# Kernel optimization log

Hardware: AMD Instinct MI355X
Metric: run time of the kernel (lower is better)

The kernel has to match this reference:

```python
import jax, jax.numpy as jnp
import numpy as np

V, D, K, NB, T = 50257, 128, 3, 8, 64
DIV_W = 2.0  # diversity_weight


def setup_inputs() -> dict:
    key = jax.random.key(0)
    k1, k2, k3 = jax.random.split(key, 3)
    tokens = jax.random.randint(k1, (T,), 0, V)
    E = jax.random.normal(k2, (V, D), jnp.float32)          # embedding table
    bubbles = 1.5 * jax.random.normal(k3, (K, NB, D), jnp.float32)  # init_spread_foam scale=1.5
    decay_base = jnp.asarray(0.8, jnp.float32)
    sensitivity = jnp.asarray(1.0, jnp.float32)
    return {"tokens": tokens, "E": E, "bubbles": bubbles,
            "decay_base": decay_base, "sensitivity": sensitivity}


def reference(tokens, E, bubbles, decay_base, sensitivity):
    d = E.shape[1]
    inv_sqrt_d = 1.0 / jnp.sqrt(jnp.asarray(d, jnp.float32))
    # normalized bubble states (pure-state directions), fixed over time
    psi = bubbles / (jnp.linalg.norm(bubbles, axis=-1, keepdims=True) + 1e-10)  # [K,NB,D]

    def step(memories, tok):
        # memories: [K, NB, D]
        x = E[tok]  # [D]
        mem_mean = memories.mean(axis=1)  # [K, D]
        mem_norm = jnp.linalg.norm(mem_mean, axis=-1) + 1e-10  # [K]
        x_norm = jnp.linalg.norm(x) + 1e-10
        cos = (mem_mean @ x) / (x_norm * mem_norm)  # [K]
        novelty = jnp.where(mem_norm > 1e-8, 1.0 - cos, 1.0)  # [K]
        decay = jax.nn.sigmoid(decay_base - jnp.abs(sensitivity) * novelty)  # [K]
        xm = x[None, :] + decay[:, None] * mem_mean  # [K, D]

        # foam forward (vectorized over K foams)
        scores = DIV_W * jnp.einsum('knd,kd->kn', bubbles, xm) * inv_sqrt_d  # [K,NB]
        w = jax.nn.softmax(scores, axis=-1)  # [K,NB]
        rho_k = jnp.einsum('kn,knd,kne->kde', w, psi, psi)  # [K,D,D] PSD, trace 1
        eq = w[..., None] * xm[:, None, :] + (1.0 - w)[..., None] * bubbles  # [K,NB,D]
        new_mem = decay[:, None, None] * memories + (1.0 - decay)[:, None, None] * eq

        rho = rho_k.mean(axis=0)  # [D,D] ensemble mixture
        eigs = jnp.clip(jnp.linalg.eigvalsh(rho), 1e-12)
        eigs = eigs / eigs.sum()
        logits = jnp.einsum('vd,de,ve->v', E, rho, E)  # born rule, [V]
        token_probs = jax.nn.softmax(logits)
        S_rho = -(eigs * jnp.clip(jnp.log(eigs), -100.0)).sum()
        H_tokens = -(token_probs * jnp.clip(jnp.log(token_probs), -100.0)).sum()
        F_tokens = H_tokens - S_rho
        logits_k = jnp.einsum('vd,kde,ve->kv', E, rho_k, E)  # [K,V]
        per_foam_probs = jax.nn.softmax(logits_k, axis=-1)
        return new_mem, (token_probs, rho, S_rho, H_tokens, F_tokens, per_foam_probs)

    mem0 = jnp.zeros((bubbles.shape[0], bubbles.shape[1], E.shape[1]), E.dtype)
    _, outs = jax.lax.scan(step, mem0, tokens)
    # outs: token_probs [T,V], rho [T,D,D], S_rho [T], H_tokens [T], F_tokens [T], per_foam_probs [T,K,V]
    return outs
```

## Files before the change

kernel.cpp:

```cpp
#include <hip/hip_runtime.h>
#include <math.h>

namespace {
constexpr int Vv  = 50257;
constexpr int Dc  = 128;
constexpr int Kc  = 3;
constexpr int NBc = 8;
constexpr int Jc  = 24;
constexpr int Tc  = 64;
constexpr int CHV = 1024;
constexpr int NCH = (Vv + CHV - 1) / CHV;
constexpr float INV_SQRT_D = 0.08838834764831845f;
constexpr float DIVW = 2.0f;

constexpr size_t WS_PSI  = 0;
constexpr size_t WS_G    = 4096;
constexpr size_t WS_BB   = 5120;
constexpr size_t WS_XN   = 6144;
constexpr size_t WS_BX   = 6400;
constexpr size_t WS_WALL = 8192;
constexpr size_t WS_PART = 12288;
constexpr size_t WS_LOGZ = 45056;
constexpr size_t WS_P2T  = 65536;

constexpr size_t OFF_TOK = 0;
constexpr size_t OFF_RHO = (size_t)Tc * Vv;
constexpr size_t OFF_S   = OFF_RHO + (size_t)Tc * Dc * Dc;
constexpr size_t OFF_H   = OFF_S + Tc;
constexpr size_t OFF_F   = OFF_H + Tc;
constexpr size_t OFF_PF  = OFF_F + Tc;
}

__device__ __forceinline__ float wsum64(float v) {
#pragma unroll
  for (int m = 1; m < 64; m <<= 1) v += __shfl_xor(v, m);
  return v;
}

__device__ __forceinline__ void comb(float& m1, float& s1, float m2, float s2) {
  float M = fmaxf(m1, m2);
  float e1 = (s1 > 0.f) ? expf(m1 - M) : 0.f;
  float e2 = (s2 > 0.f) ? expf(m2 - M) : 0.f;
  s1 = s1 * e1 + s2 * e2;
  m1 = M;
}
__device__ __forceinline__ void comb_sl(float& m1, float& s1, float& sl1,
                                        float m2, float s2, float sl2) {
  float M = fmaxf(m1, m2);
  float e1 = (s1 > 0.f) ? expf(m1 - M) : 0.f;
  float e2 = (s2 > 0.f) ? expf(m2 - M) : 0.f;
  s1 = s1 * e1 + s2 * e2;
  sl1 = sl1 * e1 + sl2 * e2;
  m1 = M;
}

__device__ __forceinline__ void logits_from_row(const float* __restrict__ p2,
                                                const float* __restrict__ wsh,
                                                int v, float& l0, float& l1, float& l2) {
  const float4* row = (const float4*)(p2 + (size_t)v * Jc);
  float4 q0 = row[0], q1 = row[1], q2 = row[2], q3 = row[3], q4 = row[4], q5 = row[5];
  l0 = 0.f; l1 = 0.f; l2 = 0.f;
  l0 += wsh[0]  * q0.x; l0 += wsh[1]  * q0.y; l0 += wsh[2]  * q0.z; l0 += wsh[3]  * q0.w;
  l0 += wsh[4]  * q1.x; l0 += wsh[5]  * q1.y; l0 += wsh[6]  * q1.z; l0 += wsh[7]  * q1.w;
  l1 += wsh[8]  * q2.x; l1 += wsh[9]  * q2.y; l1 += wsh[10] * q2.z; l1 += wsh[11] * q2.w;
  l1 += wsh[12] * q3.x; l1 += wsh[13] * q3.y; l1 += wsh[14] * q3.z; l1 += wsh[15] * q3.w;
  l2 += wsh[16] * q4.x; l2 += wsh[17] * q4.y; l2 += wsh[18] * q4.z; l2 += wsh[19] * q4.w;
  l2 += wsh[20] * q5.x; l2 += wsh[21] * q5.y; l2 += wsh[22] * q5.z; l2 += wsh[23] * q5.w;
}

__global__ void k_prep(const float* __restrict__ bub, float* __restrict__ ws) {
  __shared__ float braw[Jc * Dc];
  __shared__ float psi[Jc * Dc];
  __shared__ float nrm[Jc];
  int tid = threadIdx.x;
  for (int i = tid; i < Jc * Dc; i += 256) braw[i] = bub[i];
  __syncthreads();
  if (tid < Jc) {
    float s = 0.f;
    for (int d = 0; d < Dc; ++d) { float b = braw[tid * Dc + d]; s += b * b; }
    nrm[tid] = sqrtf(s) + 1e-10f;
  }
  __syncthreads();
  for (int i = tid; i < Jc * Dc; i += 256) {
    float v = braw[i] / nrm[i / Dc];
    psi[i] = v;
    ws[WS_PSI + i] = v;
  }
  __syncthreads();
  for (int i = tid; i < Jc * Jc; i += 256) {
    int r = i / Jc, c = i % Jc;
    float g = 0.f, b = 0.f;
    for (int d = 0; d < Dc; ++d) {
      g += psi[r * Dc + d] * psi[c * Dc + d];
      b += braw[r * Dc + d] * braw[c * Dc + d];
    }
    ws[WS_G + i] = g;
    ws[WS_BB + i] = b;
  }
}

__global__ void k_projtok(const int* __restrict__ tok, const float* __restrict__ E,
                          const float* __restrict__ bub, float* __restrict__ ws) {
  __shared__ float4 psi4[Jc][Dc / 4];
  int bid = blockIdx.x, tid = threadIdx.x;
  if (bid < Tc) {
    if (tid >= 64) return;
    int t = bid, lane = tid;
    int tk = tok[t];
    float eA = E[(size_t)tk * Dc + lane];
    float eB = E[(size_t)tk * Dc + 64 + lane];
    float xn = wsum64(eA * eA + eB * eB);
    if (lane == 0) ws[WS_XN + t] = xn;
    float p[Jc];
#pragma unroll
    for (int j = 0; j < Jc; ++j)
      p[j] = bub[j * Dc + lane] * eA + bub[j * Dc + 64 + lane] * eB;
#pragma unroll
    for (int j = 0; j < Jc; ++j) p[j] = wsum64(p[j]);
    if (lane == 0) {
#pragma unroll
      for (int j = 0; j < Jc; ++j) ws[WS_BX + (size_t)t * Jc + j] = p[j];
    }
    return;
  }
  for (int i = tid; i < Jc * Dc / 4; i += 256)
    ((float4*)psi4)[i] = ((const float4*)(ws + WS_PSI))[i];
  __syncthreads();
  int v = (bid - Tc) * 256 + tid;
  if (v >= Vv) return;
  float acc[Jc];
#pragma unroll
  for (int j = 0; j < Jc; ++j) acc[j] = 0.f;
  const float4* e4 = (const float4*)(E + (size_t)v * Dc);
  for (int d = 0; d < Dc / 4; ++d) {
    float4 e = e4[d];
#pragma unroll
    for (int j = 0; j < Jc; ++j) {
      float4 p = psi4[j][d];
      acc[j] += e.x * p.x + e.y * p.y + e.z * p.z + e.w * p.w;
    }
  }
  float* o = ws + WS_P2T + (size_t)v * Jc;
#pragma unroll
  for (int j = 0; j < Jc; ++j) o[j] = acc[j] * acc[j];
}

__global__ void k_recur(const int* __restrict__ tok, const float* __restrict__ E,
                        const float* __restrict__ bub, const float* __restrict__ pdb,
                        const float* __restrict__ psn, float* __restrict__ ws) {
  __shared__ float sBX[Tc * Jc];
  __shared__ float sXN[Tc];
  int lane = threadIdx.x;
  for (int i = lane; i < Tc * Jc; i += 64) sBX[i] = ws[WS_BX + i];
  if (lane < Tc) sXN[lane] = ws[WS_XN + lane];
  float db = pdb[0];
  float sens = fabsf(psn[0]);
  int tokv = tok[lane];
  float bubA[Jc], bubB[Jc];
#pragma unroll
  for (int j = 0; j < Jc; ++j) {
    bubA[j] = bub[j * Dc + lane];
    bubB[j] = bub[j * Dc + 64 + lane];
  }
  int jme = (lane < Jc) ? lane : (Jc - 1);
  int kme = jme >> 3;
  float BBrow[Jc];
#pragma unroll
  for (int j = 0; j < Jc; ++j) BBrow[j] = ws[WS_BB + (size_t)jme * Jc + j];
  __syncthreads();
  float mmA[Kc] = {0.f, 0.f, 0.f}, mmB[Kc] = {0.f, 0.f, 0.f};
  float BMv[Kc] = {0.f, 0.f, 0.f};
  int tk0 = __shfl(tokv, 0);
  float xA = E[(size_t)tk0 * Dc + lane];
  float xB = E[(size_t)tk0 * Dc + 64 + lane];
  for (int t = 0; t < Tc; ++t) {
    float nxA = 0.f, nxB = 0.f;
    if (t + 1 < Tc) {
      int nk = __shfl(tokv, t + 1);
      nxA = E[(size_t)nk * Dc + lane];
      nxB = E[(size_t)nk * Dc + 64 + lane];
    }
    float dk[Kc], nk2[Kc];
#pragma unroll
    for (int k = 0; k < Kc; ++k) {
      dk[k]  = wsum64(mmA[k] * xA + mmB[k] * xB);
      nk2[k] = wsum64(mmA[k] * mmA[k] + mmB[k] * mmB[k]);
    }
    float xn = sqrtf(sXN[t]) + 1e-10f;
    float dec[Kc], xmA[Kc], xmB[Kc];
#pragma unroll
    for (int k = 0; k < Kc; ++k) {
      float mn = sqrtf(nk2[k]) + 1e-10f;
      float cosv = dk[k] / (xn * mn);
      float nov = (mn > 1e-8f) ? (1.f - cosv) : 1.f;
      dec[k] = 1.f / (1.f + expf(-(db - sens * nov)));
      xmA[k] = xA + dec[k] * mmA[k];
      xmB[k] = xB + dec[k] * mmB[k];
    }
    float bxj = sBX[t * Jc + jme];
    float decS = (kme == 0) ? dec[0] : ((kme == 1) ? dec[1] : dec[2]);
    float sc = (bxj + decS * BMv[kme]) * (DIVW * INV_SQRT_D);
    float mx = sc;
    mx = fmaxf(mx, __shfl_xor(mx, 1));
    mx = fmaxf(mx, __shfl_xor(mx, 2));
    mx = fmaxf(mx, __shfl_xor(mx, 4));
    float e = expf(sc - mx);
    float ss = e;
    ss += __shfl_xor(ss, 1);
    ss += __shfl_xor(ss, 2);
    ss += __shfl_xor(ss, 4);
    float w = e / ss;
    if (lane < Jc) ws[WS_WALL + (size_t)t * Jc + lane] = w;
    float wj[Jc];
#pragma unroll
    for (int j = 0; j < Jc; ++j) wj[j] = __shfl(w, j);
#pragma unroll
    for (int k = 0; k < Kc; ++k) {
      float accA = 0.f, accB = 0.f;
#pragma unroll
      for (int n = 0; n < NBc; ++n) {
        float om = 1.f - wj[k * NBc + n];
        accA += om * bubA[k * NBc + n];
        accB += om * bubB[k * NBc + n];
      }
      float od8 = (1.f - dec[k]) * 0.125f;
      mmA[k] = dec[k] * mmA[k] + od8 * (xmA[k] + accA);
      mmB[k] = dec[k] * mmB[k] + od8 * (xmB[k] + accB);
    }
#pragma unroll
    for (int k = 0; k < Kc; ++k) {
      float bxm = bxj + dec[k] * BMv[k];
      float s2 = 0.f;
#pragma unroll
      for (int n = 0; n < NBc; ++n) s2 += (1.f - wj[k * NBc + n]) * BBrow[k * NBc + n];
      BMv[k] = dec[k] * BMv[k] + (1.f - dec[k]) * 0.125f * (bxm + s2);
    }
    xA = nxA; xB = nxB;
  }
}

__global__ void k_main(float* __restrict__ ws, float* __restrict__ out) {
  __shared__ float sh[Jc * Dc];
  __shared__ float wsh[Jc];
  __shared__ float rm[4][4], rs[4][4], rsl2[4];
  int bid = blockIdx.x, tid = threadIdx.x;

  if (bid < Tc) {
    if (tid >= 64) return;
    int t = bid, lane = tid;
    float* A = sh;
    for (int i = lane; i < Jc * Jc; i += 64) {
      int r = i / Jc, c = i % Jc;
      A[r * 25 + c] = ws[WS_G + i] *
                      sqrtf(ws[WS_WALL + (size_t)t * Jc + r] * ws[WS_WALL + (size_t)t * Jc + c]) *
                      (1.f / 3.f);
    }
    __builtin_amdgcn_wave_barrier();
    for (int sweep = 0; sweep < 7; ++sweep) {
      for (int rr = 0; rr < 23; ++rr) {
        float cv = 1.f, sv = 0.f;
        if (lane < Jc) {
          int j = lane;
          int m = (j == 23) ? rr : ((j == rr) ? 23 : (2 * rr + 23 - j) % 23);
          int lo = min(j, m), hi = max(j, m);
          float ajj = A[j * 25 + j];
          float alh = A[lo * 25 + hi];
          float amm = __shfl(ajj, m);
          float app = (j == lo) ? ajj : amm;
          float aqq = (j == lo) ? amm : ajj;
          if (fabsf(alh) > 1e-20f) {
            float th = (aqq - app) / (2.f * alh);
            float tt = 1.f / (fabsf(th) + sqrtf(1.f + th * th));
            if (th < 0.f) tt = -tt;
            cv = 1.f / sqrtf(1.f + tt * tt);
            sv = tt * cv;
          }
        }
        __builtin_amdgcn_wave_barrier();
#pragma unroll
        for (int it = 0; it < 3; ++it) {
          int b = lane + 64 * it;
          int bb = (b < 144) ? b : 143;
          int pi = bb / 12, pj = bb % 12;
          int p0, q0, p1, q1;
          if (pi == 0) { p0 = rr; q0 = 23; }
          else { int a = (rr + pi) % 23, b2 = (rr + 23 - pi) % 23; p0 = min(a, b2); q0 = max(a, b2); }
          if (pj == 0) { p1 = rr; q1 = 23; }
          else { int a = (rr + pj) % 23, b2 = (rr + 23 - pj) % 23; p1 = min(a, b2); q1 = max(a, b2); }
          float ci = __shfl(cv, p0), si = __shfl(sv, p0);
          float cj = __shfl(cv, p1), sj = __shfl(sv, p1);
          if (b < 144) {
            float m00 = A[p0 * 25 + p1], m01 = A[p0 * 25 + q1];
            float m10 = A[q0 * 25 + p1], m11 = A[q0 * 25 + q1];
            float r00 = ci * m00 - si * m10, r01 = ci * m01 - si * m11;
            float r10 = si * m00 + ci * m10, r11 = si * m01 + ci * m11;
            float o00 = cj * r00 - sj * r01, o01 = sj * r00 + cj * r01;
            float o10 = cj * r10 - sj * r11, o11 = sj * r10 + cj * r11;
            A[p0 * 25 + p1] = o00; A[p0 * 25 + q1] = o01;
            A[q0 * 25 + p1] = o10; A[q0 * 25 + q1] = o11;
          }
        }
        __builtin_amdgcn_wave_barrier();
      }
    }
    float lam = 0.f;
    if (lane < Jc) lam = fmaxf(A[lane * 25 + lane], 1e-12f);
    float tot = lam;
#pragma unroll
    for (int off = 32; off; off >>= 1) tot += __shfl_down(tot, off);
    tot = __shfl(tot, 0);
    tot += (float)(Dc - Jc) * 1e-12f;
    float term = 0.f;
    if (lane < Jc) { float p = lam / tot; term = p * logf(p); }
#pragma unroll
    for (int off = 32; off; off >>= 1) term += __shfl_down(term, off);
    if (lane == 0) {
      float pe = 1e-12f / tot;
      out[OFF_S + t] = -(term + (float)(Dc - Jc) * pe * logf(pe));
    }
    return;
  }

  if (bid < 2 * Tc) {
    int t = bid - Tc;
    float* psis = sh;
    for (int i = tid; i < Jc * Dc; i += 256) psis[i] = ws[WS_PSI + i];
    if (tid < Jc) wsh[tid] = ws[WS_WALL + (size_t)t * Jc + tid] * (1.f / 3.f);
    __syncthreads();
    int d = tid >> 1, eh = (tid & 1) * 64;
    float4 acc[16];
#pragma unroll
    for (int i = 0; i < 16; ++i) acc[i] = make_float4(0.f, 0.f, 0.f, 0.f);
    for (int j = 0; j < Jc; ++j) {
      float a = wsh[j] * psis[j * Dc + d];
      const float4* pr = (const float4*)&psis[j * Dc + eh];
#pragma unroll
      for (int i = 0; i < 16; ++i) {
        float4 p = pr[i];
        acc[i].x += a * p.x; acc[i].y += a * p.y; acc[i].z += a * p.z; acc[i].w += a * p.w;
      }
    }
    float* o = out + OFF_RHO + (size_t)t * Dc * Dc + (size_t)d * Dc + eh;
#pragma unroll
    for (int i = 0; i < 16; ++i) ((float4*)o)[i] = acc[i];
    return;
  }

  int lin = bid - 2 * Tc;
  int t = lin / NCH, ch = lin % NCH;
  if (tid < Jc) wsh[tid] = ws[WS_WALL + (size_t)t * Jc + tid];
  __syncthreads();
  float m[4] = {-INFINITY, -INFINITY, -INFINITY, -INFINITY};
  float s[4] = {0.f, 0.f, 0.f, 0.f};
  float sl = 0.f;
  const float* p2 = ws + WS_P2T;
  for (int r = 0; r < 4; ++r) {
    int v = ch * CHV + r * 256 + tid;
    if (v >= Vv) break;
    float l0, l1, l2;
    logits_from_row(p2, wsh, v, l0, l1, l2);
    float l[4] = { l0, l1, l2, (l0 + l1 + l2) * (1.f / 3.f) };
#pragma unroll
    for (int d = 0; d < 4; ++d) {
      float li = l[d];
      if (li > m[d]) {
        float e = expf(m[d] - li);
        s[d] = s[d] * e + 1.f;
        if (d == 3) sl = sl * e + li;
        m[d] = li;
      } else {
        float e = expf(li - m[d]);
        s[d] += e;
        if (d == 3) sl += e * li;
      }
    }
  }
#pragma unroll
  for (int off = 32; off; off >>= 1) {
#pragma unroll
    for (int d = 0; d < 3; ++d) {
      float om = __shfl_down(m[d], off);
      float os = __shfl_down(s[d], off);
      comb(m[d], s[d], om, os);
    }
    float om = __shfl_down(m[3], off);
    float os = __shfl_down(s[3], off);
    float osl = __shfl_down(sl, off);
    comb_sl(m[3], s[3], sl, om, os, osl);
  }
  int wv = tid >> 6, ln = tid & 63;
  if (ln == 0) {
#pragma unroll
    for (int d = 0; d < 4; ++d) { rm[wv][d] = m[d]; rs[wv][d] = s[d]; }
    rsl2[wv] = sl;
  }
  __syncthreads();
  if (tid == 0) {
    float* part = ws + WS_PART + ((size_t)t * NCH + ch) * 9;
    for (int d = 0; d < 3; ++d) {
      float M = rm[0][d], S = rs[0][d];
      for (int w2 = 1; w2 < 4; ++w2) comb(M, S, rm[w2][d], rs[w2][d]);
      part[d] = M; part[4 + d] = S;
    }
    float M = rm[0][3], S = rs[0][3], SL = rsl2[0];
    for (int w2 = 1; w2 < 4; ++w2) comb_sl(M, S, SL, rm[w2][3], rs[w2][3], rsl2[w2]);
    part[3] = M; part[7] = S; part[8] = SL;
  }
}

__global__ void k_reduce(float* __restrict__ ws, float* __restrict__ out) {
  int t = blockIdx.x, tid = threadIdx.x;
  if (tid < 4) {
    float M = -INFINITY, S = 0.f, SL = 0.f;
    for (int ch = 0; ch < NCH; ++ch) {
      const float* p = ws + WS_PART + ((size_t)t * NCH + ch) * 9;
      if (tid == 3) comb_sl(M, S, SL, p[3], p[7], p[8]);
      else          comb(M, S, p[tid], p[4 + tid]);
    }
    float lz = M + logf(S);
    ws[WS_LOGZ + (size_t)t * 4 + tid] = lz;
    if (tid == 3) {
      float H = lz - SL / S;
      float Srho = out[OFF_S + t];
      out[OFF_H + t] = H;
      out[OFF_F + t] = H - Srho;
    }
  }
}

__global__ void k_norm2(const float* __restrict__ ws, float* __restrict__ out) {
  int ch = blockIdx.x, t = blockIdx.y, tid = threadIdx.x;
  __shared__ float wsh[Jc];
  __shared__ float lzs[4];
  if (tid < Jc) wsh[tid] = ws[WS_WALL + (size_t)t * Jc + tid];
  if (tid >= 32 && tid < 36) lzs[tid - 32] = ws[WS_LOGZ + (size_t)t * 4 + (tid - 32)];
  __syncthreads();
  const float* p2 = ws + WS_P2T;
  for (int r = 0; r < 4; ++r) {
    int v = ch * CHV + r * 256 + tid;
    if (v >= Vv) break;
    float l0, l1, l2;
    logits_from_row(p2, wsh, v, l0, l1, l2);
    float l3 = (l0 + l1 + l2) * (1.f / 3.f);
    out[OFF_TOK + (size_t)t * Vv + v] = expf(l3 - lzs[3]);
    out[OFF_PF + ((size_t)t * Kc + 0) * Vv + v] = expf(l0 - lzs[0]);
    out[OFF_PF + ((size_t)t * Kc + 1) * Vv + v] = expf(l1 - lzs[1]);
    out[OFF_PF + ((size_t)t * Kc + 2) * Vv + v] = expf(l2 - lzs[2]);
  }
}

extern "C" void kernel_launch(void* const* d_in, const int* in_sizes, int n_in,
                              void* d_out, int out_size, void* d_ws, size_t ws_size,
                              hipStream_t stream) {
  const int*   tokens = (const int*)d_in[0];
  const float* E      = (const float*)d_in[1];
  const float* bub    = (const float*)d_in[2];
  const float* pdb    = (const float*)d_in[3];
  const float* psn    = (const float*)d_in[4];
  float* out = (float*)d_out;
  float* ws  = (float*)d_ws;

  k_prep<<<1, 256, 0, stream>>>(bub, ws);
  k_projtok<<<Tc + (Vv + 255) / 256, 256, 0, stream>>>(tokens, E, bub, ws);
  k_recur<<<1, 64, 0, stream>>>(tokens, E, bub, pdb, psn, ws);
  k_main<<<2 * Tc + Tc * NCH, 256, 0, stream>>>(ws, out);
  k_reduce<<<Tc, 64, 0, stream>>>(ws, out);
  k_norm2<<<dim3(NCH, Tc), 256, 0, stream>>>(ws, out);
}
```

Baseline: 445.1 us.

## Merge prep/projection kernels and fold logZ reduction into tiled normalization kernel

Merges the bubble-prep kernel into the vocab projection kernel by having every projection block recompute the normalized psi in shared memory, which removes one launch and a dependency. Removes the separate logZ reduction kernel: each normalization block now recomputes logZ for its group of 8 timesteps. That block stages a 512-token slice of the squared projections in shared memory and reuses it across those timesteps, so P2T is read from global memory far fewer times. The cost is redundant recomputation of psi and of the logZ reductions in every block, plus larger shared-memory use.

```diff
diff --git a/kernel.cpp b/kernel.cpp
--- a/kernel.cpp
+++ b/kernel.cpp
@@ -10,6 +10,10 @@
 constexpr int Tc  = 64;
 constexpr int CHV = 1024;
 constexpr int NCH = (Vv + CHV - 1) / CHV;
+constexpr int NVC = 512;
+constexpr int NNCH = (Vv + NVC - 1) / NVC;
+constexpr int NTG = 8;
+constexpr int TPG = Tc / NTG;
 constexpr float INV_SQRT_D = 0.08838834764831845f;
 constexpr float DIVW = 2.0f;
 
@@ -20,7 +24,6 @@
 constexpr size_t WS_BX   = 6400;
 constexpr size_t WS_WALL = 8192;
 constexpr size_t WS_PART = 12288;
-constexpr size_t WS_LOGZ = 45056;
 constexpr size_t WS_P2T  = 65536;
 
 constexpr size_t OFF_TOK = 0;
@@ -68,44 +71,44 @@
   l2 += wsh[20] * q5.x; l2 += wsh[21] * q5.y; l2 += wsh[22] * q5.z; l2 += wsh[23] * q5.w;
 }
 
-__global__ void k_prep(const float* __restrict__ bub, float* __restrict__ ws) {
-  __shared__ float braw[Jc * Dc];
-  __shared__ float psi[Jc * Dc];
+__global__ void k_setup(const int* __restrict__ tok, const float* __restrict__ E,
+                        const float* __restrict__ bub, float* __restrict__ ws) {
+  __shared__ __align__(16) float braw[Jc * Dc];
+  __shared__ __align__(16) float psi[Jc * Dc];
   __shared__ float nrm[Jc];
-  int tid = threadIdx.x;
-  for (int i = tid; i < Jc * Dc; i += 256) braw[i] = bub[i];
-  __syncthreads();
-  if (tid < Jc) {
-    float s = 0.f;
-    for (int d = 0; d < Dc; ++d) { float b = braw[tid * Dc + d]; s += b * b; }
-    nrm[tid] = sqrtf(s) + 1e-10f;
-  }
-  __syncthreads();
-  for (int i = tid; i < Jc * Dc; i += 256) {
-    float v = braw[i] / nrm[i / Dc];
-    psi[i] = v;
-    ws[WS_PSI + i] = v;
-  }
-  __syncthreads();
-  for (int i = tid; i < Jc * Jc; i += 256) {
-    int r = i / Jc, c = i % Jc;
-    float g = 0.f, b = 0.f;
-    for (int d = 0; d < Dc; ++d) {
-      g += psi[r * Dc + d] * psi[c * Dc + d];
-      b += braw[r * Dc + d] * braw[c * Dc + d];
-    }
-    ws[WS_G + i] = g;
-    ws[WS_BB + i] = b;
-  }
-}
-
-__global__ void k_projtok(const int* __restrict__ tok, const float* __restrict__ E,
-                          const float* __restrict__ bub, float* __restrict__ ws) {
-  __shared__ float4 psi4[Jc][Dc / 4];
   int bid = blockIdx.x, tid = threadIdx.x;
-  if (bid < Tc) {
+
+  if (bid == 0) {
+    for (int i = tid; i < Jc * Dc; i += 256) braw[i] = bub[i];
+    __syncthreads();
+    if (tid < Jc) {
+      float s = 0.f;
+      for (int d = 0; d < Dc; ++d) { float b = braw[tid * Dc + d]; s += b * b; }
+      nrm[tid] = sqrtf(s) + 1e-10f;
+    }
+    __syncthreads();
+    for (int i = tid; i < Jc * Dc; i += 256) {
+      float v = braw[i] / nrm[i / Dc];
+      psi[i] = v;
+      ws[WS_PSI + i] = v;
+    }
+    __syncthreads();
+    for (int i = tid; i < Jc * Jc; i += 256) {
+      int r = i / Jc, c = i % Jc;
+      float g = 0.f, b = 0.f;
+      for (int d = 0; d < Dc; ++d) {
+        g += psi[r * Dc + d] * psi[c * Dc + d];
+        b += braw[r * Dc + d] * braw[c * Dc + d];
+      }
+      ws[WS_G + i] = g;
+      ws[WS_BB + i] = b;
+    }
+    return;
+  }
+
+  if (bid <= Tc) {
     if (tid >= 64) return;
-    int t = bid, lane = tid;
+    int t = bid - 1, lane = tid;
     int tk = tok[t];
     float eA = E[(size_t)tk * Dc + lane];
     float eB = E[(size_t)tk * Dc + 64 + lane];
@@ -123,20 +126,29 @@
     }
     return;
   }
-  for (int i = tid; i < Jc * Dc / 4; i += 256)
-    ((float4*)psi4)[i] = ((const float4*)(ws + WS_PSI))[i];
-  __syncthreads();
-  int v = (bid - Tc) * 256 + tid;
+
+  for (int i = tid; i < Jc * Dc; i += 256) braw[i] = bub[i];
+  __syncthreads();
+  if (tid < Jc) {
+    float s = 0.f;
+    for (int d = 0; d < Dc; ++d) { float b = braw[tid * Dc + d]; s += b * b; }
+    nrm[tid] = sqrtf(s) + 1e-10f;
+  }
+  __syncthreads();
+  for (int i = tid; i < Jc * Dc; i += 256) psi[i] = braw[i] / nrm[i / Dc];
+  __syncthreads();
+  int v = (bid - Tc - 1) * 256 + tid;
   if (v >= Vv) return;
   float acc[Jc];
 #pragma unroll
   for (int j = 0; j < Jc; ++j) acc[j] = 0.f;
   const float4* e4 = (const float4*)(E + (size_t)v * Dc);
+  const float4* p4 = (const float4*)psi;
   for (int d = 0; d < Dc / 4; ++d) {
     float4 e = e4[d];
 #pragma unroll
     for (int j = 0; j < Jc; ++j) {
-      float4 p = psi4[j][d];
+      float4 p = p4[j * (Dc / 4) + d];
       acc[j] += e.x * p.x + e.y * p.y + e.z * p.z + e.w * p.w;
     }
   }
@@ -408,44 +420,79 @@
   }
 }
 
-__global__ void k_reduce(float* __restrict__ ws, float* __restrict__ out) {
-  int t = blockIdx.x, tid = threadIdx.x;
-  if (tid < 4) {
+__global__ void k_norm2(const float* __restrict__ ws, float* __restrict__ out) {
+  __shared__ float p2s[Jc][NVC];
+  __shared__ float wshA[TPG][Jc];
+  __shared__ float lzsA[TPG][4];
+  int chv = blockIdx.x, tg = blockIdx.y, tid = threadIdx.x;
+  int v0 = chv * NVC;
+  int t0 = tg * TPG;
+
+#pragma unroll
+  for (int rr = 0; rr < 2; ++rr) {
+    int vl = tid * 2 + rr;
+    int v = v0 + vl;
+    if (v < Vv) {
+      const float4* row = (const float4*)(ws + WS_P2T + (size_t)v * Jc);
+      float4 q0 = row[0], q1 = row[1], q2 = row[2], q3 = row[3], q4 = row[4], q5 = row[5];
+      p2s[0][vl] = q0.x;  p2s[1][vl] = q0.y;  p2s[2][vl] = q0.z;  p2s[3][vl] = q0.w;
+      p2s[4][vl] = q1.x;  p2s[5][vl] = q1.y;  p2s[6][vl] = q1.z;  p2s[7][vl] = q1.w;
+      p2s[8][vl] = q2.x;  p2s[9][vl] = q2.y;  p2s[10][vl] = q2.z; p2s[11][vl] = q2.w;
+      p2s[12][vl] = q3.x; p2s[13][vl] = q3.y; p2s[14][vl] = q3.z; p2s[15][vl] = q3.w;
+      p2s[16][vl] = q4.x; p2s[17][vl] = q4.y; p2s[18][vl] = q4.z; p2s[19][vl] = q4.w;
+      p2s[20][vl] = q5.x; p2s[21][vl] = q5.y; p2s[22][vl] = q5.z; p2s[23][vl] = q5.w;
+    }
+  }
+  if (tid < TPG * Jc)
+    wshA[tid / Jc][tid % Jc] = ws[WS_WALL + (size_t)(t0 + tid / Jc) * Jc + (tid % Jc)];
+  if (tid >= 192 && tid < 192 + TPG * 4) {
+    int p = tid - 192;
+    int tt = p >> 2, d = p & 3;
+    int t = t0 + tt;
     float M = -INFINITY, S = 0.f, SL = 0.f;
     for (int ch = 0; ch < NCH; ++ch) {
-      const float* p = ws + WS_PART + ((size_t)t * NCH + ch) * 9;
-      if (tid == 3) comb_sl(M, S, SL, p[3], p[7], p[8]);
-      else          comb(M, S, p[tid], p[4 + tid]);
+      const float* pp = ws + WS_PART + ((size_t)t * NCH + ch) * 9;
+      if (d == 3) comb_sl(M, S, SL, pp[3], pp[7], pp[8]);
+      else        comb(M, S, pp[d], pp[4 + d]);
     }
     float lz = M + logf(S);
-    ws[WS_LOGZ + (size_t)t * 4 + tid] = lz;
-    if (tid == 3) {
+    lzsA[tt][d] = lz;
+    if (d == 3 && chv == 0) {
       float H = lz - SL / S;
       float Srho = out[OFF_S + t];
       out[OFF_H + t] = H;
       out[OFF_F + t] = H - Srho;
     }
   }
-}
-
-__global__ void k_norm2(const float* __restrict__ ws, float* __restrict__ out) {
-  int ch = blockIdx.x, t = blockIdx.y, tid = threadIdx.x;
-  __shared__ float wsh[Jc];
-  __shared__ float lzs[4];
-  if (tid < Jc) wsh[tid] = ws[WS_WALL + (size_t)t * Jc + tid];
-  if (tid >= 32 && tid < 36) lzs[tid - 32] = ws[WS_LOGZ + (size_t)t * 4 + (tid - 32)];
-  __syncthreads();
-  const float* p2 = ws + WS_P2T;
-  for (int r = 0; r < 4; ++r) {
-    int v = ch * CHV + r * 256 + tid;
-    if (v >= Vv) break;
-    float l0, l1, l2;
-    logits_from_row(p2, wsh, v, l0, l1, l2);
-    float l3 = (l0 + l1 + l2) * (1.f / 3.f);
-    out[OFF_TOK + (size_t)t * Vv + v] = expf(l3 - lzs[3]);
-    out[OFF_PF + ((size_t)t * Kc + 0) * Vv + v] = expf(l0 - lzs[0]);
-    out[OFF_PF + ((size_t)t * Kc + 1) * Vv + v] = expf(l1 - lzs[1]);
-    out[OFF_PF + ((size_t)t * Kc + 2) * Vv + v] = expf(l2 - lzs[2]);
+  __syncthreads();
+
+  for (int tt = 0; tt < TPG; ++tt) {
+    int t = t0 + tt;
+    float lz0 = lzsA[tt][0], lz1 = lzsA[tt][1], lz2 = lzsA[tt][2], lz3 = lzsA[tt][3];
+#pragma unroll
+    for (int rr = 0; rr < 2; ++rr) {
+      int vl = tid + rr * 256;
+      int v = v0 + vl;
+      if (v >= Vv) continue;
+      float l0 = 0.f, l1 = 0.f, l2 = 0.f;
+      l0 += wshA[tt][0]  * p2s[0][vl];  l0 += wshA[tt][1]  * p2s[1][vl];
+      l0 += wshA[tt][2]  * p2s[2][vl];  l0 += wshA[tt][3]  * p2s[3][vl];
+      l0 += wshA[tt][4]  * p2s[4][vl];  l0 += wshA[tt][5]  * p2s[5][vl];
+      l0 += wshA[tt][6]  * p2s[6][vl];  l0 += wshA[tt][7]  * p2s[7][vl];
+      l1 += wshA[tt][8]  * p2s[8][vl];  l1 += wshA[tt][9]  * p2s[9][vl];
+      l1 += wshA[tt][10] * p2s[10][vl]; l1 += wshA[tt][11] * p2s[11][vl];
+      l1 += wshA[tt][12] * p2s[12][vl]; l1 += wshA[tt][13] * p2s[13][vl];
+      l1 += wshA[tt][14] * p2s[14][vl]; l1 += wshA[tt][15] * p2s[15][vl];
+      l2 += wshA[tt][16] * p2s[16][vl]; l2 += wshA[tt][17] * p2s[17][vl];
+      l2 += wshA[tt][18] * p2s[18][vl]; l2 += wshA[tt][19] * p2s[19][vl];
+      l2 += wshA[tt][20] * p2s[20][vl]; l2 += wshA[tt][21] * p2s[21][vl];
+      l2 += wshA[tt][22] * p2s[22][vl]; l2 += wshA[tt][23] * p2s[23][vl];
+      float l3 = (l0 + l1 + l2) * (1.f / 3.f);
+      out[OFF_TOK + (size_t)t * Vv + v] = expf(l3 - lz3);
+      out[OFF_PF + ((size_t)t * Kc + 0) * Vv + v] = expf(l0 - lz0);
+      out[OFF_PF + ((size_t)t * Kc + 1) * Vv + v] = expf(l1 - lz1);
+      out[OFF_PF + ((size_t)t * Kc + 2) * Vv + v] = expf(l2 - lz2);
+    }
   }
 }
 
@@ -460,10 +507,8 @@
   float* out = (float*)d_out;
   float* ws  = (float*)d_ws;
 
-  k_prep<<<1, 256, 0, stream>>>(bub, ws);
-  k_projtok<<<Tc + (Vv + 255) / 256, 256, 0, stream>>>(tokens, E, bub, ws);
+  k_setup<<<1 + Tc + (Vv + 255) / 256, 256, 0, stream>>>(tokens, E, bub, ws);
   k_recur<<<1, 64, 0, stream>>>(tokens, E, bub, pdb, psn, ws);
   k_main<<<2 * Tc + Tc * NCH, 256, 0, stream>>>(ws, out);
-  k_reduce<<<Tc, 64, 0, stream>>>(ws, out);
-  k_norm2<<<dim3(NCH, Tc), 256, 0, stream>>>(ws, out);
-}
+  k_norm2<<<dim3(NNCH, NTG), 256, 0, stream>>>(ws, out);
+}
```

After: 457.6 us. 2.8% more time.

## Merge prep into projection kernel and fold reduce into final normalize kernel

Applied to the files above, without the earlier changes.

Fuses the single-block prep kernel into the projection kernel: each projection block recomputes the normalized bubble directions locally instead of waiting on a separate launch. The Jacobi eigen-solve and entropy computation move into the final kernel, which also does the global logZ combine. Each normalize block redundantly reduces all chunk partials itself, removing the separate reduce kernel. This cuts six launches to four and removes serial single-block stages, in exchange for redundant per-block recomputation of psi and of the partial reductions.

```diff
diff --git a/kernel.cpp b/kernel.cpp
--- a/kernel.cpp
+++ b/kernel.cpp
@@ -20,7 +20,6 @@
 constexpr size_t WS_BX   = 6400;
 constexpr size_t WS_WALL = 8192;
 constexpr size_t WS_PART = 12288;
-constexpr size_t WS_LOGZ = 45056;
 constexpr size_t WS_P2T  = 65536;
 
 constexpr size_t OFF_TOK = 0;
@@ -68,44 +67,44 @@
   l2 += wsh[20] * q5.x; l2 += wsh[21] * q5.y; l2 += wsh[22] * q5.z; l2 += wsh[23] * q5.w;
 }
 
-__global__ void k_prep(const float* __restrict__ bub, float* __restrict__ ws) {
-  __shared__ float braw[Jc * Dc];
-  __shared__ float psi[Jc * Dc];
+__global__ void k_setup(const int* __restrict__ tok, const float* __restrict__ E,
+                        const float* __restrict__ bub, float* __restrict__ ws) {
+  __shared__ __align__(16) float braw[Jc * Dc];
+  __shared__ __align__(16) float psi[Jc * Dc];
   __shared__ float nrm[Jc];
-  int tid = threadIdx.x;
-  for (int i = tid; i < Jc * Dc; i += 256) braw[i] = bub[i];
-  __syncthreads();
-  if (tid < Jc) {
-    float s = 0.f;
-    for (int d = 0; d < Dc; ++d) { float b = braw[tid * Dc + d]; s += b * b; }
-    nrm[tid] = sqrtf(s) + 1e-10f;
-  }
-  __syncthreads();
-  for (int i = tid; i < Jc * Dc; i += 256) {
-    float v = braw[i] / nrm[i / Dc];
-    psi[i] = v;
-    ws[WS_PSI + i] = v;
-  }
-  __syncthreads();
-  for (int i = tid; i < Jc * Jc; i += 256) {
-    int r = i / Jc, c = i % Jc;
-    float g = 0.f, b = 0.f;
-    for (int d = 0; d < Dc; ++d) {
-      g += psi[r * Dc + d] * psi[c * Dc + d];
-      b += braw[r * Dc + d] * braw[c * Dc + d];
-    }
-    ws[WS_G + i] = g;
-    ws[WS_BB + i] = b;
-  }
-}
-
-__global__ void k_projtok(const int* __restrict__ tok, const float* __restrict__ E,
-                          const float* __restrict__ bub, float* __restrict__ ws) {
-  __shared__ float4 psi4[Jc][Dc / 4];
   int bid = blockIdx.x, tid = threadIdx.x;
-  if (bid < Tc) {
+
+  if (bid == 0) {
+    for (int i = tid; i < Jc * Dc; i += 256) braw[i] = bub[i];
+    __syncthreads();
+    if (tid < Jc) {
+      float s = 0.f;
+      for (int d = 0; d < Dc; ++d) { float b = braw[tid * Dc + d]; s += b * b; }
+      nrm[tid] = sqrtf(s) + 1e-10f;
+    }
+    __syncthreads();
+    for (int i = tid; i < Jc * Dc; i += 256) {
+      float v = braw[i] / nrm[i / Dc];
+      psi[i] = v;
+      ws[WS_PSI + i] = v;
+    }
+    __syncthreads();
+    for (int i = tid; i < Jc * Jc; i += 256) {
+      int r = i / Jc, c = i % Jc;
+      float g = 0.f, b = 0.f;
+      for (int d = 0; d < Dc; ++d) {
+        g += psi[r * Dc + d] * psi[c * Dc + d];
+        b += braw[r * Dc + d] * braw[c * Dc + d];
+      }
+      ws[WS_G + i] = g;
+      ws[WS_BB + i] = b;
+    }
+    return;
+  }
+
+  if (bid <= Tc) {
     if (tid >= 64) return;
-    int t = bid, lane = tid;
+    int t = bid - 1, lane = tid;
     int tk = tok[t];
     float eA = E[(size_t)tk * Dc + lane];
     float eB = E[(size_t)tk * Dc + 64 + lane];
@@ -123,20 +122,29 @@
     }
     return;
   }
-  for (int i = tid; i < Jc * Dc / 4; i += 256)
-    ((float4*)psi4)[i] = ((const float4*)(ws + WS_PSI))[i];
-  __syncthreads();
-  int v = (bid - Tc) * 256 + tid;
+
+  for (int i = tid; i < Jc * Dc; i += 256) braw[i] = bub[i];
+  __syncthreads();
+  if (tid < Jc) {
+    float s = 0.f;
+    for (int d = 0; d < Dc; ++d) { float b = braw[tid * Dc + d]; s += b * b; }
+    nrm[tid] = sqrtf(s) + 1e-10f;
+  }
+  __syncthreads();
+  for (int i = tid; i < Jc * Dc; i += 256) psi[i] = braw[i] / nrm[i / Dc];
+  __syncthreads();
+  int v = (bid - Tc - 1) * 256 + tid;
   if (v >= Vv) return;
   float acc[Jc];
 #pragma unroll
   for (int j = 0; j < Jc; ++j) acc[j] = 0.f;
   const float4* e4 = (const float4*)(E + (size_t)v * Dc);
+  const float4* p4 = (const float4*)psi;
   for (int d = 0; d < Dc / 4; ++d) {
     float4 e = e4[d];
 #pragma unroll
     for (int j = 0; j < Jc; ++j) {
-      float4 p = psi4[j][d];
+      float4 p = p4[j * (Dc / 4) + d];
       acc[j] += e.x * p.x + e.y * p.y + e.z * p.z + e.w * p.w;
     }
   }
@@ -239,16 +247,108 @@
   }
 }
 
-__global__ void k_main(float* __restrict__ ws, float* __restrict__ out) {
+__global__ void k_part(float* __restrict__ ws, float* __restrict__ out) {
   __shared__ float sh[Jc * Dc];
   __shared__ float wsh[Jc];
   __shared__ float rm[4][4], rs[4][4], rsl2[4];
   int bid = blockIdx.x, tid = threadIdx.x;
 
   if (bid < Tc) {
+    int t = bid;
+    float* psis = sh;
+    for (int i = tid; i < Jc * Dc; i += 256) psis[i] = ws[WS_PSI + i];
+    if (tid < Jc) wsh[tid] = ws[WS_WALL + (size_t)t * Jc + tid] * (1.f / 3.f);
+    __syncthreads();
+    int d = tid >> 1, eh = (tid & 1) * 64;
+    float4 acc[16];
+#pragma unroll
+    for (int i = 0; i < 16; ++i) acc[i] = make_float4(0.f, 0.f, 0.f, 0.f);
+    for (int j = 0; j < Jc; ++j) {
+      float a = wsh[j] * psis[j * Dc + d];
+      const float4* pr = (const float4*)&psis[j * Dc + eh];
+#pragma unroll
+      for (int i = 0; i < 16; ++i) {
+        float4 p = pr[i];
+        acc[i].x += a * p.x; acc[i].y += a * p.y; acc[i].z += a * p.z; acc[i].w += a * p.w;
+      }
+    }
+    float* o = out + OFF_RHO + (size_t)t * Dc * Dc + (size_t)d * Dc + eh;
+#pragma unroll
+    for (int i = 0; i < 16; ++i) ((float4*)o)[i] = acc[i];
+    return;
+  }
+
+  int lin = bid - Tc;
+  int t = lin / NCH, ch = lin % NCH;
+  if (tid < Jc) wsh[tid] = ws[WS_WALL + (size_t)t * Jc + tid];
+  __syncthreads();
+  float m[4] = {-INFINITY, -INFINITY, -INFINITY, -INFINITY};
+  float s[4] = {0.f, 0.f, 0.f, 0.f};
+  float sl = 0.f;
+  const float* p2 = ws + WS_P2T;
+  for (int r = 0; r < 4; ++r) {
+    int v = ch * CHV + r * 256 + tid;
+    if (v >= Vv) break;
+    float l0, l1, l2;
+    logits_from_row(p2, wsh, v, l0, l1, l2);
+    float l[4] = { l0, l1, l2, (l0 + l1 + l2) * (1.f / 3.f) };
+#pragma unroll
+    for (int d = 0; d < 4; ++d) {
+      float li = l[d];
+      if (li > m[d]) {
+        float e = expf(m[d] - li);
+        s[d] = s[d] * e + 1.f;
+        if (d == 3) sl = sl * e + li;
+        m[d] = li;
+      } else {
+        float e = expf(li - m[d]);
+        s[d] += e;
+        if (d == 3) sl += e * li;
+      }
+    }
+  }
+#pragma unroll
+  for (int off = 32; off; off >>= 1) {
+#pragma unroll
+    for (int d = 0; d < 3; ++d) {
+      float om = __shfl_down(m[d], off);
+      float os = __shfl_down(s[d], off);
+      comb(m[d], s[d], om, os);
+    }
+    float om = __shfl_down(m[3], off);
+    float os = __shfl_down(s[3], off);
+    float osl = __shfl_down(sl, off);
+    comb_sl(m[3], s[3], sl, om, os, osl);
+  }
+  int wv = tid >> 6, ln = tid & 63;
+  if (ln == 0) {
+#pragma unroll
+    for (int d = 0; d < 4; ++d) { rm[wv][d] = m[d]; rs[wv][d] = s[d]; }
+    rsl2[wv] = sl;
+  }
+  __syncthreads();
+  if (tid == 0) {
+    float* part = ws + WS_PART + ((size_t)t * NCH + ch) * 9;
+    for (int d = 0; d < 3; ++d) {
+      float M = rm[0][d], S = rs[0][d];
+      for (int w2 = 1; w2 < 4; ++w2) comb(M, S, rm[w2][d], rs[w2][d]);
+      part[d] = M; part[4 + d] = S;
+    }
+    float M = rm[0][3], S = rs[0][3], SL = rsl2[0];
+    for (int w2 = 1; w2 < 4; ++w2) comb_sl(M, S, SL, rm[w2][3], rs[w2][3], rsl2[w2]);
+    part[3] = M; part[7] = S; part[8] = SL;
+  }
+}
+
+__global__ void k_final(float* __restrict__ ws, float* __restrict__ out) {
+  __shared__ float A[Jc * 25];
+  __shared__ float wsh[Jc];
+  __shared__ float lzs[4];
+  int bid = blockIdx.x, tid = threadIdx.x;
+
+  if (bid < Tc) {
     if (tid >= 64) return;
     int t = bid, lane = tid;
-    float* A = sh;
     for (int i = lane; i < Jc * Jc; i += 64) {
       int r = i / Jc, c = i % Jc;
       A[r * 25 + c] = ws[WS_G + i] *
@@ -316,125 +416,36 @@
     for (int off = 32; off; off >>= 1) term += __shfl_down(term, off);
     if (lane == 0) {
       float pe = 1e-12f / tot;
-      out[OFF_S + t] = -(term + (float)(Dc - Jc) * pe * logf(pe));
+      float Srho = -(term + (float)(Dc - Jc) * pe * logf(pe));
+      out[OFF_S + t] = Srho;
+      float M = -INFINITY, S = 0.f, SL = 0.f;
+      for (int ch = 0; ch < NCH; ++ch) {
+        const float* pp = ws + WS_PART + ((size_t)t * NCH + ch) * 9;
+        comb_sl(M, S, SL, pp[3], pp[7], pp[8]);
+      }
+      float lz = M + logf(S);
+      float H = lz - SL / S;
+      out[OFF_H + t] = H;
+      out[OFF_F + t] = H - Srho;
     }
     return;
   }
 
-  if (bid < 2 * Tc) {
-    int t = bid - Tc;
-    float* psis = sh;
-    for (int i = tid; i < Jc * Dc; i += 256) psis[i] = ws[WS_PSI + i];
-    if (tid < Jc) wsh[tid] = ws[WS_WALL + (size_t)t * Jc + tid] * (1.f / 3.f);
-    __syncthreads();
-    int d = tid >> 1, eh = (tid & 1) * 64;
-    float4 acc[16];
-#pragma unroll
-    for (int i = 0; i < 16; ++i) acc[i] = make_float4(0.f, 0.f, 0.f, 0.f);
-    for (int j = 0; j < Jc; ++j) {
-      float a = wsh[j] * psis[j * Dc + d];
-      const float4* pr = (const float4*)&psis[j * Dc + eh];
-#pragma unroll
-      for (int i = 0; i < 16; ++i) {
-        float4 p = pr[i];
-        acc[i].x += a * p.x; acc[i].y += a * p.y; acc[i].z += a * p.z; acc[i].w += a * p.w;
-      }
-    }
-    float* o = out + OFF_RHO + (size_t)t * Dc * Dc + (size_t)d * Dc + eh;
-#pragma unroll
-    for (int i = 0; i < 16; ++i) ((float4*)o)[i] = acc[i];
-    return;
-  }
-
-  int lin = bid - 2 * Tc;
+  int lin = bid - Tc;
   int t = lin / NCH, ch = lin % NCH;
   if (tid < Jc) wsh[tid] = ws[WS_WALL + (size_t)t * Jc + tid];
-  __syncthreads();
-  float m[4] = {-INFINITY, -INFINITY, -INFINITY, -INFINITY};
-  float s[4] = {0.f, 0.f, 0.f, 0.f};
-  float sl = 0.f;
-  const float* p2 = ws + WS_P2T;
-  for (int r = 0; r < 4; ++r) {
-    int v = ch * CHV + r * 256 + tid;
-    if (v >= Vv) break;
-    float l0, l1, l2;
-    logits_from_row(p2, wsh, v, l0, l1, l2);
-    float l[4] = { l0, l1, l2, (l0 + l1 + l2) * (1.f / 3.f) };
-#pragma unroll
-    for (int d = 0; d < 4; ++d) {
-      float li = l[d];
-      if (li > m[d]) {
-        float e = expf(m[d] - li);
-        s[d] = s[d] * e + 1.f;
-        if (d == 3) sl = sl * e + li;
-        m[d] = li;
-      } else {
-        float e = expf(li - m[d]);
-        s[d] += e;
-        if (d == 3) sl += e * li;
-      }
-    }
-  }
-#pragma unroll
-  for (int off = 32; off; off >>= 1) {
-#pragma unroll
-    for (int d = 0; d < 3; ++d) {
-      float om = __shfl_down(m[d], off);
-      float os = __shfl_down(s[d], off);
-      comb(m[d], s[d], om, os);
-    }
-    float om = __shfl_down(m[3], off);
-    float os = __shfl_down(s[3], off);
-    float osl = __shfl_down(sl, off);
-    comb_sl(m[3], s[3], sl, om, os, osl);
-  }
-  int wv = tid >> 6, ln = tid & 63;
-  if (ln == 0) {
-#pragma unroll
-    for (int d = 0; d < 4; ++d) { rm[wv][d] = m[d]; rs[wv][d] = s[d]; }
-    rsl2[wv] = sl;
-  }
-  __syncthreads();
-  if (tid == 0) {
-    float* part = ws + WS_PART + ((size_t)t * NCH + ch) * 9;
-    for (int d = 0; d < 3; ++d) {
-      float M = rm[0][d], S = rs[0][d];
-      for (int w2 = 1; w2 < 4; ++w2) comb(M, S, rm[w2][d], rs[w2][d]);
-      part[d] = M; part[4 + d] = S;
-    }
-    float M = rm[0][3], S = rs[0][3], SL = rsl2[0];
-    for (int w2 = 1; w2 < 4; ++w2) comb_sl(M, S, SL, rm[w2][3], rs[w2][3], rsl2[w2]);
-    part[3] = M; part[7] = S; part[8] = SL;
-  }
-}
-
-__global__ void k_reduce(float* __restrict__ ws, float* __restrict__ out) {
-  int t = blockIdx.x, tid = threadIdx.x;
-  if (tid < 4) {
+  if (tid >= 32 && tid < 36) {
+    int d = tid - 32;
     float M = -INFINITY, S = 0.f, SL = 0.f;
-    for (int ch = 0; ch < NCH; ++ch) {
-      const float* p = ws + WS_PART + ((size_t)t * NCH + ch) * 9;
-      if (tid == 3) comb_sl(M, S, SL, p[3], p[7], p[8]);
-      else          comb(M, S, p[tid], p[4 + tid]);
-    }
-    float lz = M + logf(S);
-    ws[WS_LOGZ + (size_t)t * 4 + tid] = lz;
-    if (tid == 3) {
-      float H = lz - SL / S;
-      float Srho = out[OFF_S + t];
-      out[OFF_H + t] = H;
-      out[OFF_F + t] = H - Srho;
-    }
-  }
-}
-
-__global__ void k_norm2(const float* __restrict__ ws, float* __restrict__ out) {
-  int ch = blockIdx.x, t = blockIdx.y, tid = threadIdx.x;
-  __shared__ float wsh[Jc];
-  __shared__ float lzs[4];
-  if (tid < Jc) wsh[tid] = ws[WS_WALL + (size_t)t * Jc + tid];
-  if (tid >= 32 && tid < 36) lzs[tid - 32] = ws[WS_LOGZ + (size_t)t * 4 + (tid - 32)];
-  __syncthreads();
+    for (int c2 = 0; c2 < NCH; ++c2) {
+      const float* pp = ws + WS_PART + ((size_t)t * NCH + c2) * 9;
+      if (d == 3) comb_sl(M, S, SL, pp[3], pp[7], pp[8]);
+      else        comb(M, S, pp[d], pp[4 + d]);
+    }
+    lzs[d] = M + logf(S);
+  }
+  __syncthreads();
+  float lz0 = lzs[0], lz1 = lzs[1], lz2 = lzs[2], lz3 = lzs[3];
   const float* p2 = ws + WS_P2T;
   for (int r = 0; r < 4; ++r) {
     int v = ch * CHV + r * 256 + tid;
@@ -442,10 +453,10 @@
     float l0, l1, l2;
     logits_from_row(p2, wsh, v, l0, l1, l2);
     float l3 = (l0 + l1 + l2) * (1.f / 3.f);
-    out[OFF_TOK + (size_t)t * Vv + v] = expf(l3 - lzs[3]);
-    out[OFF_PF + ((size_t)t * Kc + 0) * Vv + v] = expf(l0 - lzs[0]);
-    out[OFF_PF + ((size_t)t * Kc + 1) * Vv + v] = expf(l1 - lzs[1]);
-    out[OFF_PF + ((size_t)t * Kc + 2) * Vv + v] = expf(l2 - lzs[2]);
+    out[OFF_TOK + (size_t)t * Vv + v] = expf(l3 - lz3);
+    out[OFF_PF + ((size_t)t * Kc + 0) * Vv + v] = expf(l0 - lz0);
+    out[OFF_PF + ((size_t)t * Kc + 1) * Vv + v] = expf(l1 - lz1);
+    out[OFF_PF + ((size_t)t * Kc + 2) * Vv + v] = expf(l2 - lz2);
   }
 }
 
@@ -460,10 +471,8 @@
   float* out = (float*)d_out;
   float* ws  = (float*)d_ws;
 
-  k_prep<<<1, 256, 0, stream>>>(bub, ws);
-  k_projtok<<<Tc + (Vv + 255) / 256, 256, 0, stream>>>(tokens, E, bub, ws);
+  k_setup<<<1 + Tc + (Vv + 255) / 256, 256, 0, stream>>>(tokens, E, bub, ws);
   k_recur<<<1, 64, 0, stream>>>(tokens, E, bub, pdb, psn, ws);
-  k_main<<<2 * Tc + Tc * NCH, 256, 0, stream>>>(ws, out);
-  k_reduce<<<Tc, 64, 0, stream>>>(ws, out);
-  k_norm2<<<dim3(NCH, Tc), 256, 0, stream>>>(ws, out);
-}
+  k_part<<<Tc + Tc * NCH, 256, 0, stream>>>(ws, out);
+  k_final<<<Tc + Tc * NCH, 256, 0, stream>>>(ws, out);
+}
```

After: 428.9 us. 1.04x faster.
